# Kernel optimization log

Measured on AMD Instinct MI355X. Metric: run time of the kernel, lower is better.

## Reference

```python
import jax, jax.numpy as jnp
import numpy as np

N, C_IN, G, C_OUT, K = 500000, 128, 256, 128, 27
EPS_LN = 1e-6
EPS_GRN = 1e-6


def setup_inputs() -> dict:
    key = jax.random.key(0)
    ks = jax.random.split(key, 12)
    s = 0.02
    return {
        "x": jax.random.normal(ks[0], (N, C_IN), dtype=jnp.float32),
        "neighbor_idx": jax.random.randint(ks[1], (N, K), 0, N, dtype=jnp.int32),
        "W1": jax.random.normal(ks[2], (C_IN, G), dtype=jnp.float32) * s,
        "b1": jax.random.normal(ks[3], (G,), dtype=jnp.float32) * s,
        "ln_g": jnp.ones((G,), dtype=jnp.float32),
        "ln_b": jnp.zeros((G,), dtype=jnp.float32),
        "dw_w": jax.random.normal(ks[4], (K, G), dtype=jnp.float32) * s,
        "dw_b": jax.random.normal(ks[5], (G,), dtype=jnp.float32) * s,
        "W2": jax.random.normal(ks[6], (G, C_OUT), dtype=jnp.float32) * s,
        "b2": jax.random.normal(ks[7], (C_OUT,), dtype=jnp.float32) * s,
        "grn_g": jax.random.normal(ks[8], (1, C_OUT), dtype=jnp.float32) * s,
        "grn_b": jax.random.normal(ks[9], (1, C_OUT), dtype=jnp.float32) * s,
    }


def _block(x, neighbor_idx, W1, b1, ln_g, ln_b, dw_w, dw_b, W2, b2, grn_g, grn_b):
    # 1x1 sparse conv == per-point linear: [N, C_in] -> [N, G]
    h = x @ W1 + b1
    # LayerNorm over channels, eps=1e-6
    mu = jnp.mean(h, axis=-1, keepdims=True)
    var = jnp.mean(jnp.square(h - mu), axis=-1, keepdims=True)
    h = (h - mu) * jax.lax.rsqrt(var + EPS_LN) * ln_g + ln_b
    # Depthwise 3^3 sparse conv: gather K=27 neighbors, per-channel weights
    def tap(acc, k):
        return acc + h[neighbor_idx[:, k]] * dw_w[k], None
    acc, _ = jax.lax.scan(tap, jnp.zeros_like(h), jnp.arange(K))
    h = acc + dw_b
    # 1x1 projection [N, G] -> [N, C_out]
    h = h @ W2 + b2
    # GELU (torch default: exact erf form)
    h = jax.nn.gelu(h, approximate=False)
    # GRN: global response norm over all points, per channel
    Gx = jnp.linalg.norm(h, axis=0, keepdims=True)          # [1, C_out]
    Nx = Gx / (jnp.mean(Gx, axis=-1, keepdims=True) + EPS_GRN)
    h = grn_g * (h * Nx) + grn_b + h
    # residual
    return h + x


def reference(x, neighbor_idx, W1, b1, ln_g, ln_b, dw_w, dw_b, W2, b2, grn_g, grn_b):
    return _block(x, neighbor_idx, W1, b1, ln_g, ln_b, dw_w, dw_b, W2, b2, grn_g, grn_b)
```

## Files before the change

### kernel.cpp

```cpp
#include <hip/hip_runtime.h>
#include <cstdint>
#include <cstddef>

#define NPTS 500000
#define CIN  128
#define GCH  256
#define COUT 128
#define KTAP 27

typedef __attribute__((ext_vector_type(4))) float    f32x4;
typedef __attribute__((ext_vector_type(2))) float    f32x2;
typedef __attribute__((ext_vector_type(8))) short    s16x8;
typedef __attribute__((ext_vector_type(4))) uint32_t u32x4;
typedef __attribute__((ext_vector_type(2))) uint32_t u32x2;

__device__ __forceinline__ unsigned short f2bf(float f) {
  union { float f; uint32_t u; } v; v.f = f;
  uint32_t r = v.u + 0x7FFFu + ((v.u >> 16) & 1u);
  return (unsigned short)(r >> 16);
}
__device__ __forceinline__ float bf2f(unsigned short h) {
  union { uint32_t u; float f; } v; v.u = ((uint32_t)h) << 16;
  return v.f;
}

__global__ __launch_bounds__(256) void k_prep(
    const float* __restrict__ W1, const float* __restrict__ W2,
    unsigned short* __restrict__ W1t, uint8_t* __restrict__ W2t8,
    float* __restrict__ sums) {
  int b = blockIdx.x, t = threadIdx.x;
  if (b == 0 && t < COUT) sums[t] = 0.f;
  int gt = (b & 15) * 256 + t;
  int grp = gt >> 6, lane = gt & 63;
  int l15 = lane & 15, l4 = lane >> 4;
  if (b < 16) {
    int f = grp >> 2, s = grp & 3;
    int col = f * 16 + l15, k0 = s * 32 + l4 * 8;
    unsigned short* dst = W1t + gt * 8;
#pragma unroll
    for (int j = 0; j < 8; ++j) dst[j] = f2bf(W1[(size_t)(k0 + j) * GCH + col]);
  } else {
    int f = grp >> 3, s = grp & 7;
    int col = f * 16 + l15, k0 = s * 32 + l4 * 8;
    float w[8];
#pragma unroll
    for (int e = 0; e < 8; ++e) w[e] = W2[(size_t)(k0 + e) * COUT + col];
    int lo = __builtin_amdgcn_cvt_pk_fp8_f32(w[0], w[1], 0, false);
    lo = __builtin_amdgcn_cvt_pk_fp8_f32(w[2], w[3], lo, true);
    int hi = __builtin_amdgcn_cvt_pk_fp8_f32(w[4], w[5], 0, false);
    hi = __builtin_amdgcn_cvt_pk_fp8_f32(w[6], w[7], hi, true);
    u32x2 q = {(uint32_t)lo, (uint32_t)hi};
    *(u32x2*)(W2t8 + gt * 8) = q;
  }
}

__global__ __launch_bounds__(512) void k_gemm1_ln(
    const float* __restrict__ x, const unsigned short* __restrict__ W1t,
    const float* __restrict__ b1, const float* __restrict__ ln_g,
    const float* __restrict__ ln_b, uint8_t* __restrict__ h1A,
    uint8_t* __restrict__ h1B) {
  __shared__ unsigned short Wl[4096 * 8];
  __shared__ float lnbuf[8][16][2];
  int tid = threadIdx.x, lane = tid & 63, wv = tid >> 6;
  int l15 = lane & 15, l4 = lane >> 4;
  int wr = wv >> 1, wc = wv & 1;
  long rowbase = (long)blockIdx.x * 64;

#pragma unroll
  for (int i = 0; i < 8; ++i) {
    int off = (i * 512 + tid) * 8;
    *(s16x8*)&Wl[off] = *(const s16x8*)&W1t[off];
  }

  long gr = rowbase + wr * 16 + l15;
  bool ok = gr < NPTS;
  const float* xp = x + gr * CIN + l4 * 8;
  s16x8 a[4];
#pragma unroll
  for (int s = 0; s < 4; ++s) {
    f32x4 v0 = {0.f, 0.f, 0.f, 0.f}, v1 = {0.f, 0.f, 0.f, 0.f};
    if (ok) {
      v0 = *(const f32x4*)(xp + s * 32);
      v1 = *(const f32x4*)(xp + s * 32 + 4);
    }
    s16x8 t;
    t[0] = (short)f2bf(v0[0]); t[1] = (short)f2bf(v0[1]);
    t[2] = (short)f2bf(v0[2]); t[3] = (short)f2bf(v0[3]);
    t[4] = (short)f2bf(v1[0]); t[5] = (short)f2bf(v1[1]);
    t[6] = (short)f2bf(v1[2]); t[7] = (short)f2bf(v1[3]);
    a[s] = t;
  }
  __syncthreads();

  f32x4 acc[8];
#pragma unroll
  for (int f = 0; f < 8; ++f) acc[f] = (f32x4){0.f, 0.f, 0.f, 0.f};
#pragma unroll
  for (int f = 0; f < 8; ++f)
#pragma unroll
    for (int s = 0; s < 4; ++s) {
      s16x8 w = *(const s16x8*)&Wl[(((wc * 8 + f) * 4 + s) * 64 + lane) * 8];
      acc[f] = __builtin_amdgcn_mfma_f32_16x16x32_bf16(w, a[s], acc[f], 0, 0, 0);
    }

  float s1 = 0.f, s2 = 0.f;
#pragma unroll
  for (int f = 0; f < 8; ++f) {
    f32x4 bb = *(const f32x4*)(b1 + wc * 128 + f * 16 + l4 * 4);
#pragma unroll
    for (int j = 0; j < 4; ++j) {
      float v = acc[f][j] + bb[j];
      acc[f][j] = v;
      s1 += v; s2 += v * v;
    }
  }
  s1 += __shfl_xor(s1, 16); s1 += __shfl_xor(s1, 32);
  s2 += __shfl_xor(s2, 16); s2 += __shfl_xor(s2, 32);
  if (lane < 16) { lnbuf[wv][l15][0] = s1; lnbuf[wv][l15][1] = s2; }
  __syncthreads();
  float t1 = s1 + lnbuf[wv ^ 1][l15][0];
  float t2 = s2 + lnbuf[wv ^ 1][l15][1];
  float mu = t1 * (1.f / GCH);
  float var = t2 * (1.f / GCH) - mu * mu;
  float rs = rsqrtf(var + 1e-6f);

  long p = gr;
  uint8_t* dp = (wc ? h1B : h1A) + p * 128 + l4 * 4;
#pragma unroll
  for (int f = 0; f < 8; ++f) {
    f32x4 g4 = *(const f32x4*)(ln_g + wc * 128 + f * 16 + l4 * 4);
    f32x4 b4 = *(const f32x4*)(ln_b + wc * 128 + f * 16 + l4 * 4);
    float v0 = (acc[f][0] - mu) * rs * g4[0] + b4[0];
    float v1 = (acc[f][1] - mu) * rs * g4[1] + b4[1];
    float v2 = (acc[f][2] - mu) * rs * g4[2] + b4[2];
    float v3 = (acc[f][3] - mu) * rs * g4[3] + b4[3];
    int w0 = __builtin_amdgcn_cvt_pk_fp8_f32(v0, v1, 0, false);
    w0 = __builtin_amdgcn_cvt_pk_fp8_f32(v2, v3, w0, true);
    if (ok) *(uint32_t*)(dp + f * 16) = (uint32_t)w0;
  }
}

__global__ __launch_bounds__(256) void k_dw(
    const uint8_t* __restrict__ h1h, const int* __restrict__ nbr,
    const float* __restrict__ dw_w, const float* __restrict__ dw_b,
    uint8_t* __restrict__ h2f8, int choff) {
  __shared__ float wf[KTAP * 8 * 20];
  __shared__ int idxl[64 * KTAP];
  int tid = threadIdx.x, lane = tid & 63, wv = tid >> 6;
  int li = lane & 7, g = lane >> 3;

  if (tid < KTAP * 8) {
    int k = tid >> 3, l = tid & 7;
    const float* wp = dw_w + k * GCH + choff + l * 16;
    float* d = &wf[(k * 8 + l) * 20];
#pragma unroll
    for (int e = 0; e < 16; e += 4) *(f32x4*)&d[e] = *(const f32x4*)&wp[e];
  }
  size_t pblk = (size_t)blockIdx.x * 64;
  for (int i = tid; i < 64 * KTAP; i += 256) {
    size_t gi = pblk * KTAP + i;
    idxl[i] = (gi < (size_t)NPTS * KTAP) ? __builtin_nontemporal_load(nbr + gi) : 0;
  }
  __syncthreads();

  f32x2 bias[8];
#pragma unroll
  for (int d = 0; d < 4; ++d) {
    f32x4 b4 = *(const f32x4*)(dw_b + choff + li * 16 + d * 4);
    bias[2 * d]     = (f32x2){b4[0], b4[1]};
    bias[2 * d + 1] = (f32x2){b4[2], b4[3]};
  }
  int boff = li * 16;

#pragma unroll
  for (int it = 0; it < 2; ++it) {
    int pl = it * 32 + wv * 8 + g;
    size_t p = pblk + pl;
    f32x2 acc[8];
#pragma unroll
    for (int i = 0; i < 8; ++i) acc[i] = bias[i];
#pragma unroll
    for (int k = 0; k < KTAP; ++k) {
      int row = idxl[pl * KTAP + k];
      u32x4 hv = *(const u32x4*)(h1h + ((size_t)(uint32_t)row << 7) + boff);
#pragma unroll
      for (int j = 0; j < 4; ++j) {
        f32x4 w4 = *(const f32x4*)&wf[(k * 8 + li) * 20 + j * 4];
        f32x2 lo = __builtin_amdgcn_cvt_pk_f32_fp8(hv[j], false);
        f32x2 hi = __builtin_amdgcn_cvt_pk_f32_fp8(hv[j], true);
        acc[2 * j]     += lo * (f32x2){w4[0], w4[1]};
        acc[2 * j + 1] += hi * (f32x2){w4[2], w4[3]};
      }
    }
    u32x4 o;
#pragma unroll
    for (int j = 0; j < 4; ++j) {
      int u = __builtin_amdgcn_cvt_pk_fp8_f32(acc[2 * j][0], acc[2 * j][1], 0, false);
      u = __builtin_amdgcn_cvt_pk_fp8_f32(acc[2 * j + 1][0], acc[2 * j + 1][1], u, true);
      o[j] = (uint32_t)u;
    }
    if (p < NPTS)
      __builtin_nontemporal_store(o, (u32x4*)(h2f8 + p * GCH + choff + boff));
  }
}

__global__ __launch_bounds__(512) void k_gemm2(
    const uint8_t* __restrict__ h2f8, const uint8_t* __restrict__ W2t8,
    const float* __restrict__ b2, unsigned short* __restrict__ h3,
    float* __restrict__ sums) {
  __shared__ uint8_t Al[128][GCH + 16];
  __shared__ float ssum[COUT];
  int tid = threadIdx.x, lane = tid & 63, wv = tid >> 6;
  int l15 = lane & 15, l4 = lane >> 4;
  long rowbase = (long)blockIdx.x * 128;
  if (tid < COUT) ssum[tid] = 0.f;
  {
    int ar = tid >> 2, ac = (tid & 3) * 64;
    long gr = rowbase + ar;
    const uint8_t* sp = h2f8 + gr * GCH + ac;
    bool ok = gr < NPTS;
    u32x4 z = {0, 0, 0, 0};
#pragma unroll
    for (int u = 0; u < 4; ++u) {
      u32x4 v = z;
      if (ok) v = __builtin_nontemporal_load((const u32x4*)(sp + u * 16));
      *(u32x4*)&Al[ar][ac + u * 16] = v;
    }
  }
  __syncthreads();

  f32x4 acc[8];
#pragma unroll
  for (int f = 0; f < 8; ++f) acc[f] = (f32x4){0.f, 0.f, 0.f, 0.f};
  long aa[8];
#pragma unroll
  for (int s = 0; s < 8; ++s)
    aa[s] = *(const long*)&Al[wv * 16 + l15][s * 32 + l4 * 8];
#pragma unroll
  for (int f = 0; f < 8; ++f)
#pragma unroll
    for (int s = 0; s < 8; ++s) {
      long bb = *(const long*)&W2t8[((f * 8 + s) * 64 + lane) * 8];
      acc[f] = __builtin_amdgcn_mfma_f32_16x16x32_fp8_fp8(aa[s], bb, acc[f], 0, 0, 0);
    }
#pragma unroll
  for (int f = 0; f < 8; ++f) {
    int col = f * 16 + l15;
    float bbv = b2[col];
    float ps = 0.f;
#pragma unroll
    for (int j = 0; j < 4; ++j) {
      long r = rowbase + wv * 16 + l4 * 4 + j;
      float v = acc[f][j] + bbv;
      float g = 0.5f * v * (1.f + erff(v * 0.70710678118654752f));
      if (r < NPTS) {
        h3[r * COUT + col] = f2bf(g);
        ps += g * g;
      }
    }
    ps += __shfl_xor(ps, 16);
    ps += __shfl_xor(ps, 32);
    if (l4 == 0) atomicAdd(&ssum[col], ps);
  }
  __syncthreads();
  if (tid < COUT) atomicAdd(&sums[tid], ssum[tid]);
}

__global__ void k_grn(const float* __restrict__ sums, const float* __restrict__ grn_g,
                      const float* __restrict__ grn_b, float* __restrict__ sAB) {
  __shared__ float gx[COUT];
  __shared__ float mean_s;
  int t = threadIdx.x;
  float g = sqrtf(sums[t]);
  gx[t] = g;
  __syncthreads();
  if (t == 0) {
    float s = 0.f;
    for (int i = 0; i < COUT; ++i) s += gx[i];
    mean_s = s * (1.f / COUT);
  }
  __syncthreads();
  float nx = g / (mean_s + 1e-6f);
  sAB[t] = grn_g[t] * nx + 1.f;
  sAB[COUT + t] = grn_b[t];
}

__global__ __launch_bounds__(256) void k_final(
    const unsigned short* __restrict__ h3, const float* __restrict__ x,
    const float* __restrict__ sAB, float* __restrict__ out) {
  long q = (long)blockIdx.x * 256 + threadIdx.x;
  long idx = q * 4;
  int c0 = (int)(idx & (COUT - 1));
  f32x4 sA = *(const f32x4*)(sAB + c0);
  f32x4 sB = *(const f32x4*)(sAB + COUT + c0);
  ushort4 hv = *(const ushort4*)(h3 + idx);
  f32x4 xv = __builtin_nontemporal_load((const f32x4*)(x + idx));
  f32x4 r;
  r[0] = bf2f(hv.x) * sA[0] + sB[0] + xv[0];
  r[1] = bf2f(hv.y) * sA[1] + sB[1] + xv[1];
  r[2] = bf2f(hv.z) * sA[2] + sB[2] + xv[2];
  r[3] = bf2f(hv.w) * sA[3] + sB[3] + xv[3];
  __builtin_nontemporal_store(r, (f32x4*)(out + idx));
}

extern "C" void kernel_launch(void* const* d_in, const int* in_sizes, int n_in,
                              void* d_out, int out_size, void* d_ws, size_t ws_size,
                              hipStream_t stream) {
  const float* x     = (const float*)d_in[0];
  const int*   nbr   = (const int*)d_in[1];
  const float* W1    = (const float*)d_in[2];
  const float* b1    = (const float*)d_in[3];
  const float* ln_g  = (const float*)d_in[4];
  const float* ln_b  = (const float*)d_in[5];
  const float* dw_w  = (const float*)d_in[6];
  const float* dw_b  = (const float*)d_in[7];
  const float* W2    = (const float*)d_in[8];
  const float* b2    = (const float*)d_in[9];
  const float* grn_g = (const float*)d_in[10];
  const float* grn_b = (const float*)d_in[11];
  float* out = (float*)d_out;

  char* ws = (char*)d_ws;
  const size_t HALF = (size_t)NPTS * 128;
  uint8_t* h1A        = (uint8_t*)ws;
  uint8_t* h1B        = (uint8_t*)(ws + HALF);
  unsigned short* h3  = (unsigned short*)(ws + 2 * HALF);
  size_t off = (size_t)NPTS * GCH * 2;
  unsigned short* W1t = (unsigned short*)(ws + off);
  uint8_t* W2t8       = (uint8_t*)(ws + off + 65536);
  float* sums         = (float*)(ws + off + 65536 + 32768);
  float* sAB          = (float*)(ws + off + 65536 + 32768 + 512);
  uint8_t* h2f8       = (uint8_t*)d_out;

  k_prep<<<32, 256, 0, stream>>>(W1, W2, W1t, W2t8, sums);
  k_gemm1_ln<<<(NPTS + 63) / 64, 512, 0, stream>>>(x, W1t, b1, ln_g, ln_b, h1A, h1B);
  k_dw<<<(NPTS + 63) / 64, 256, 0, stream>>>(h1A, nbr, dw_w, dw_b, h2f8, 0);
  k_dw<<<(NPTS + 63) / 64, 256, 0, stream>>>(h1B, nbr, dw_w, dw_b, h2f8, 128);
  k_gemm2<<<(NPTS + 127) / 128, 512, 0, stream>>>(h2f8, W2t8, b2, h3, sums);
  k_grn<<<1, COUT, 0, stream>>>(sums, grn_g, grn_b, sAB);
  k_final<<<(NPTS * COUT / 4) / 256, 256, 0, stream>>>(h3, x, sAB, out);
}
```

Before: 941.8 us.

## Fuse depthwise gather conv into GEMM2 and unify h1 into one fp8 buffer

The two channel-half depthwise gather kernels and the second GEMM are merged into one kernel. The depthwise result goes into LDS and feeds the fp8 MFMA directly, so the h2 intermediate is never written to or read back from global memory. h1 is now stored as a single interleaved 256-byte row per point, so each neighbour gather reads the full row in one pass instead of two passes over half-width buffers, and the h3 stores are marked nontemporal. The cost is higher LDS use per block (weights, indices and the A tile), which may lower occupancy for the latency-bound gather phase.

```diff
diff --git a/kernel.cpp b/kernel.cpp
--- a/kernel.cpp
+++ b/kernel.cpp
@@ -57,8 +57,7 @@
 __global__ __launch_bounds__(512) void k_gemm1_ln(
     const float* __restrict__ x, const unsigned short* __restrict__ W1t,
     const float* __restrict__ b1, const float* __restrict__ ln_g,
-    const float* __restrict__ ln_b, uint8_t* __restrict__ h1A,
-    uint8_t* __restrict__ h1B) {
+    const float* __restrict__ ln_b, uint8_t* __restrict__ h1f8) {
   __shared__ unsigned short Wl[4096 * 8];
   __shared__ float lnbuf[8][16][2];
   int tid = threadIdx.x, lane = tid & 63, wv = tid >> 6;
@@ -124,8 +123,7 @@
   float var = t2 * (1.f / GCH) - mu * mu;
   float rs = rsqrtf(var + 1e-6f);
 
-  long p = gr;
-  uint8_t* dp = (wc ? h1B : h1A) + p * 128 + l4 * 4;
+  uint8_t* dp = h1f8 + gr * GCH + wc * 128 + l4 * 4;
 #pragma unroll
   for (int f = 0; f < 8; ++f) {
     f32x4 g4 = *(const f32x4*)(ln_g + wc * 128 + f * 16 + l4 * 4);
@@ -140,91 +138,66 @@
   }
 }
 
-__global__ __launch_bounds__(256) void k_dw(
-    const uint8_t* __restrict__ h1h, const int* __restrict__ nbr,
+__global__ __launch_bounds__(512) void k_dwg2(
+    const uint8_t* __restrict__ h1f8, const int* __restrict__ nbr,
     const float* __restrict__ dw_w, const float* __restrict__ dw_b,
-    uint8_t* __restrict__ h2f8, int choff) {
-  __shared__ float wf[KTAP * 8 * 20];
-  __shared__ int idxl[64 * KTAP];
-  int tid = threadIdx.x, lane = tid & 63, wv = tid >> 6;
-  int li = lane & 7, g = lane >> 3;
-
-  if (tid < KTAP * 8) {
-    int k = tid >> 3, l = tid & 7;
-    const float* wp = dw_w + k * GCH + choff + l * 16;
-    float* d = &wf[(k * 8 + l) * 20];
-#pragma unroll
-    for (int e = 0; e < 16; e += 4) *(f32x4*)&d[e] = *(const f32x4*)&wp[e];
-  }
-  size_t pblk = (size_t)blockIdx.x * 64;
-  for (int i = tid; i < 64 * KTAP; i += 256) {
-    size_t gi = pblk * KTAP + i;
-    idxl[i] = (gi < (size_t)NPTS * KTAP) ? __builtin_nontemporal_load(nbr + gi) : 0;
-  }
-  __syncthreads();
-
-  f32x2 bias[8];
-#pragma unroll
-  for (int d = 0; d < 4; ++d) {
-    f32x4 b4 = *(const f32x4*)(dw_b + choff + li * 16 + d * 4);
-    bias[2 * d]     = (f32x2){b4[0], b4[1]};
-    bias[2 * d + 1] = (f32x2){b4[2], b4[3]};
-  }
-  int boff = li * 16;
-
-#pragma unroll
-  for (int it = 0; it < 2; ++it) {
-    int pl = it * 32 + wv * 8 + g;
-    size_t p = pblk + pl;
-    f32x2 acc[8];
-#pragma unroll
-    for (int i = 0; i < 8; ++i) acc[i] = bias[i];
-#pragma unroll
-    for (int k = 0; k < KTAP; ++k) {
-      int row = idxl[pl * KTAP + k];
-      u32x4 hv = *(const u32x4*)(h1h + ((size_t)(uint32_t)row << 7) + boff);
-#pragma unroll
-      for (int j = 0; j < 4; ++j) {
-        f32x4 w4 = *(const f32x4*)&wf[(k * 8 + li) * 20 + j * 4];
-        f32x2 lo = __builtin_amdgcn_cvt_pk_f32_fp8(hv[j], false);
-        f32x2 hi = __builtin_amdgcn_cvt_pk_f32_fp8(hv[j], true);
-        acc[2 * j]     += lo * (f32x2){w4[0], w4[1]};
-        acc[2 * j + 1] += hi * (f32x2){w4[2], w4[3]};
-      }
-    }
-    u32x4 o;
-#pragma unroll
-    for (int j = 0; j < 4; ++j) {
-      int u = __builtin_amdgcn_cvt_pk_fp8_f32(acc[2 * j][0], acc[2 * j][1], 0, false);
-      u = __builtin_amdgcn_cvt_pk_fp8_f32(acc[2 * j + 1][0], acc[2 * j + 1][1], u, true);
-      o[j] = (uint32_t)u;
-    }
-    if (p < NPTS)
-      __builtin_nontemporal_store(o, (u32x4*)(h2f8 + p * GCH + choff + boff));
-  }
-}
-
-__global__ __launch_bounds__(512) void k_gemm2(
-    const uint8_t* __restrict__ h2f8, const uint8_t* __restrict__ W2t8,
-    const float* __restrict__ b2, unsigned short* __restrict__ h3,
-    float* __restrict__ sums) {
+    const uint8_t* __restrict__ W2t8, const float* __restrict__ b2,
+    unsigned short* __restrict__ h3, float* __restrict__ sums) {
+  __shared__ float wf[KTAP * 4 * 16 * 4];
+  __shared__ int idxl[128 * KTAP];
   __shared__ uint8_t Al[128][GCH + 16];
   __shared__ float ssum[COUT];
   int tid = threadIdx.x, lane = tid & 63, wv = tid >> 6;
   int l15 = lane & 15, l4 = lane >> 4;
-  long rowbase = (long)blockIdx.x * 128;
+  size_t pblk = (size_t)blockIdx.x * 128;
+
+  for (int u = tid; u < KTAP * 64; u += 512) {
+    int g = u >> 4, ld = u & 15, k = g >> 2, j = g & 3;
+    *(f32x4*)&wf[u * 4] = *(const f32x4*)(dw_w + k * GCH + ld * 16 + j * 4);
+  }
   if (tid < COUT) ssum[tid] = 0.f;
+  for (int i = tid; i < 128 * KTAP; i += 512) {
+    size_t gi = pblk * KTAP + i;
+    idxl[i] = (gi < (size_t)NPTS * KTAP) ? __builtin_nontemporal_load(nbr + gi) : 0;
+  }
+  __syncthreads();
+
   {
-    int ar = tid >> 2, ac = (tid & 3) * 64;
-    long gr = rowbase + ar;
-    const uint8_t* sp = h2f8 + gr * GCH + ac;
-    bool ok = gr < NPTS;
-    u32x4 z = {0, 0, 0, 0};
-#pragma unroll
-    for (int u = 0; u < 4; ++u) {
-      u32x4 v = z;
-      if (ok) v = __builtin_nontemporal_load((const u32x4*)(sp + u * 16));
-      *(u32x4*)&Al[ar][ac + u * 16] = v;
+    f32x2 bias[8];
+#pragma unroll
+    for (int d = 0; d < 4; ++d) {
+      f32x4 b4 = *(const f32x4*)(dw_b + l15 * 16 + d * 4);
+      bias[2 * d]     = (f32x2){b4[0], b4[1]};
+      bias[2 * d + 1] = (f32x2){b4[2], b4[3]};
+    }
+    int coff = l15 * 16;
+#pragma unroll
+    for (int it = 0; it < 4; ++it) {
+      int pl = it * 32 + wv * 4 + l4;
+      f32x2 acc[8];
+#pragma unroll
+      for (int i = 0; i < 8; ++i) acc[i] = bias[i];
+#pragma unroll
+      for (int k = 0; k < KTAP; ++k) {
+        int row = idxl[pl * KTAP + k];
+        u32x4 hv = *(const u32x4*)(h1f8 + ((size_t)(uint32_t)row << 8) + coff);
+#pragma unroll
+        for (int j = 0; j < 4; ++j) {
+          f32x4 w4 = *(const f32x4*)&wf[((k * 4 + j) * 16 + l15) * 4];
+          f32x2 lo = __builtin_amdgcn_cvt_pk_f32_fp8(hv[j], false);
+          f32x2 hi = __builtin_amdgcn_cvt_pk_f32_fp8(hv[j], true);
+          acc[2 * j]     += lo * (f32x2){w4[0], w4[1]};
+          acc[2 * j + 1] += hi * (f32x2){w4[2], w4[3]};
+        }
+      }
+      u32x4 o;
+#pragma unroll
+      for (int j = 0; j < 4; ++j) {
+        int u = __builtin_amdgcn_cvt_pk_fp8_f32(acc[2 * j][0], acc[2 * j][1], 0, false);
+        u = __builtin_amdgcn_cvt_pk_fp8_f32(acc[2 * j + 1][0], acc[2 * j + 1][1], u, true);
+        o[j] = (uint32_t)u;
+      }
+      *(u32x4*)&Al[pl][coff] = o;
     }
   }
   __syncthreads();
@@ -250,11 +223,11 @@
     float ps = 0.f;
 #pragma unroll
     for (int j = 0; j < 4; ++j) {
-      long r = rowbase + wv * 16 + l4 * 4 + j;
+      long r = (long)pblk + wv * 16 + l4 * 4 + j;
       float v = acc[f][j] + bbv;
       float g = 0.5f * v * (1.f + erff(v * 0.70710678118654752f));
       if (r < NPTS) {
-        h3[r * COUT + col] = f2bf(g);
+        __builtin_nontemporal_store(f2bf(g), &h3[r * COUT + col]);
         ps += g * g;
       }
     }
@@ -321,22 +294,17 @@
   float* out = (float*)d_out;
 
   char* ws = (char*)d_ws;
-  const size_t HALF = (size_t)NPTS * 128;
-  uint8_t* h1A        = (uint8_t*)ws;
-  uint8_t* h1B        = (uint8_t*)(ws + HALF);
-  unsigned short* h3  = (unsigned short*)(ws + 2 * HALF);
+  uint8_t* h1f8       = (uint8_t*)ws;
+  unsigned short* h3  = (unsigned short*)(ws + (size_t)NPTS * GCH);
   size_t off = (size_t)NPTS * GCH * 2;
   unsigned short* W1t = (unsigned short*)(ws + off);
   uint8_t* W2t8       = (uint8_t*)(ws + off + 65536);
   float* sums         = (float*)(ws + off + 65536 + 32768);
   float* sAB          = (float*)(ws + off + 65536 + 32768 + 512);
-  uint8_t* h2f8       = (uint8_t*)d_out;
 
   k_prep<<<32, 256, 0, stream>>>(W1, W2, W1t, W2t8, sums);
-  k_gemm1_ln<<<(NPTS + 63) / 64, 512, 0, stream>>>(x, W1t, b1, ln_g, ln_b, h1A, h1B);
-  k_dw<<<(NPTS + 63) / 64, 256, 0, stream>>>(h1A, nbr, dw_w, dw_b, h2f8, 0);
-  k_dw<<<(NPTS + 63) / 64, 256, 0, stream>>>(h1B, nbr, dw_w, dw_b, h2f8, 128);
-  k_gemm2<<<(NPTS + 127) / 128, 512, 0, stream>>>(h2f8, W2t8, b2, h3, sums);
+  k_gemm1_ln<<<(NPTS + 63) / 64, 512, 0, stream>>>(x, W1t, b1, ln_g, ln_b, h1f8);
+  k_dwg2<<<(NPTS + 127) / 128, 512, 0, stream>>>(h1f8, nbr, dw_w, dw_b, W2t8, b2, h3, sums);
   k_grn<<<1, COUT, 0, stream>>>(sums, grn_g, grn_b, sAB);
   k_final<<<(NPTS * COUT / 4) / 256, 256, 0, stream>>>(h3, x, sAB, out);
 }
```

New measurement: 882.9 us. -6.3%, faster.
